# Kernel tuning notes

Hardware: AMD Instinct MI355X
Metric: run time of the kernel (lower is better)

## Reference

```python
import jax, jax.numpy as jnp
import numpy as np
import math

B, S, E = 2, 2048, 1024
H, HD = 16, 64  # num_heads, head_size


def setup_inputs() -> dict:
    key = jax.random.key(0)
    ks = jax.random.split(key, 9)
    sc = 1.0 / math.sqrt(HD)
    return {
        "x": jax.random.normal(ks[0], (B, S, E), dtype=jnp.float32),
        "Wq_w": jax.random.normal(ks[1], (HD, HD), dtype=jnp.float32) * sc,
        "Wq_b": jax.random.normal(ks[2], (HD,), dtype=jnp.float32) * 0.02,
        "Wk_w": jax.random.normal(ks[3], (HD, HD), dtype=jnp.float32) * sc,
        "Wk_b": jax.random.normal(ks[4], (HD,), dtype=jnp.float32) * 0.02,
        "Wv_w": jax.random.normal(ks[5], (HD, HD), dtype=jnp.float32) * sc,
        "Wv_b": jax.random.normal(ks[6], (HD,), dtype=jnp.float32) * 0.02,
        "proj_w": jax.random.normal(ks[7], (E, E), dtype=jnp.float32) * (1.0 / math.sqrt(E)),
        "proj_b": jax.random.normal(ks[8], (E,), dtype=jnp.float32) * 0.02,
    }


def reference(x, Wq_w, Wq_b, Wk_w, Wk_b, Wv_w, Wv_b, proj_w, proj_b):
    b, s, _ = x.shape
    xh = x.reshape(b, s, H, HD)  # split heads; QKV linears act per-head (shared weights)
    # torch Linear: y = x @ W.T + b
    q = jnp.einsum('bshd,ed->bhse', xh, Wq_w) + Wq_b  # [B,H,S,HD]
    k = jnp.einsum('bshd,ed->bhse', xh, Wk_w) + Wk_b
    v = jnp.einsum('bshd,ed->bhse', xh, Wv_w) + Wv_b
    scores = jnp.einsum('bhqd,bhkd->bhqk', q, k) / math.sqrt(HD)
    causal = jnp.tril(jnp.ones((s, s), dtype=bool))
    scores = jnp.where(causal, scores, jnp.float32(-1e20))
    attn = jax.nn.softmax(scores, axis=-1)  # attn_dropout p=0 (eval)
    out = jnp.einsum('bhqk,bhkd->bqhd', attn, v).reshape(b, s, H * HD)
    out = out @ proj_w.T + proj_b  # resid_dropout p=0 (eval)
    return out
```

## Files before the change

kernel.cpp:

```cpp
#include <hip/hip_runtime.h>
#include <hip/hip_bf16.h>

#define B_ 2
#define S_ 2048
#define E_ 1024
#define H_ 16
#define HD_ 64
#define T_ (B_ * S_)

typedef short bf16x8 __attribute__((ext_vector_type(8)));
typedef short bf16x4 __attribute__((ext_vector_type(4)));
typedef float f32x4 __attribute__((ext_vector_type(4)));

__device__ __forceinline__ short f2bf(float f) {
  union { float f; unsigned u; } v;
  v.f = f;
  unsigned r = v.u + 0x7fffu + ((v.u >> 16) & 1u);
  return (short)(r >> 16);
}

__device__ __forceinline__ void gll16(const void* g, void* l) {
  __builtin_amdgcn_global_load_lds(
      (const __attribute__((address_space(1))) unsigned int*)g,
      (__attribute__((address_space(3))) unsigned int*)l, 16, 0, 0);
}


__global__ __launch_bounds__(256) void qkv_conv_kernel(
    const float* __restrict__ x,
    const float* __restrict__ wq, const float* __restrict__ bq,
    const float* __restrict__ wk, const float* __restrict__ bk,
    const float* __restrict__ wv, const float* __restrict__ bv,
    short* __restrict__ Q, short* __restrict__ KV,
    const float* __restrict__ pw, short* __restrict__ pwb) {
  const int tid = threadIdx.x;
  if (blockIdx.x >= 512) {
    int i = ((blockIdx.x - 512) * 256 + tid) * 4;
    float4 f = *(const float4*)(pw + i);
    bf16x4 o;
    o[0] = f2bf(f.x); o[1] = f2bf(f.y); o[2] = f2bf(f.z); o[3] = f2bf(f.w);
    *(bf16x4*)(pwb + i) = o;
    return;
  }
  __shared__ short Xs[64][136];
  __shared__ short Ws[192][72];
  __shared__ short Qt[64][68], Kt[64][68], Vt[64][68];

  const int bid = blockIdx.x;
  const int tb = bid >> 3, hg = bid & 7;
  const int s0 = (tb * 64) & (S_ - 1);
  const int kt = s0 >> 6;
  const int bb = (tb * 64) >> 11;
  const int wave = tid >> 6, lane = tid & 63;
  const int lrow = lane & 15, quad = lane >> 4;

#pragma unroll
  for (int i = 0; i < 8; i++) {
    int c = tid + 256 * i;
    int row = c >> 5, col4 = c & 31;
    float4 f = *(const float4*)(x + ((long)(tb * 64 + row)) * E_ + hg * 128 + col4 * 4);
    bf16x4 o;
    o[0] = f2bf(f.x); o[1] = f2bf(f.y); o[2] = f2bf(f.z); o[3] = f2bf(f.w);
    *(bf16x4*)&Xs[row][col4 * 4] = o;
  }
#pragma unroll
  for (int m = 0; m < 3; m++) {
    const float* w = (m == 0) ? wq : (m == 1) ? wk : wv;
#pragma unroll
    for (int i = 0; i < 4; i++) {
      int c = tid + 256 * i;
      int row = m * 64 + (c >> 4), col = (c & 15) * 4;
      float4 f = *(const float4*)(w + (long)c * 4);
      bf16x4 o;
      o[0] = f2bf(f.x); o[1] = f2bf(f.y); o[2] = f2bf(f.z); o[3] = f2bf(f.w);
      *(bf16x4*)&Ws[row][col] = o;
    }
  }
  float bias[12];
#pragma unroll
  for (int nb = 0; nb < 12; nb++) {
    int sel = nb >> 2;
    int e = ((nb & 3) * 16) + lrow;
    bias[nb] = ((sel == 0) ? bq : (sel == 1) ? bk : bv)[e];
  }
  __syncthreads();

  bf16x8 bf0[12], bf1[12];
#pragma unroll
  for (int nb = 0; nb < 12; nb++) {
    bf0[nb] = *(bf16x8*)&Ws[nb * 16 + lrow][quad * 8];
    bf1[nb] = *(bf16x8*)&Ws[nb * 16 + lrow][32 + quad * 8];
  }

  const float QSCALE = 0.125f * 1.44269504089f;
  for (int hl = 0; hl < 2; hl++) {
    const int h = hg * 2 + hl;
    bf16x8 a0 = *(bf16x8*)&Xs[wave * 16 + lrow][hl * 64 + quad * 8];
    bf16x8 a1 = *(bf16x8*)&Xs[wave * 16 + lrow][hl * 64 + 32 + quad * 8];
#pragma unroll
    for (int nb = 0; nb < 12; nb++) {
      f32x4 acc = {0.f, 0.f, 0.f, 0.f};
      acc = __builtin_amdgcn_mfma_f32_16x16x32_bf16(a0, bf0[nb], acc, 0, 0, 0);
      acc = __builtin_amdgcn_mfma_f32_16x16x32_bf16(a1, bf1[nb], acc, 0, 0, 0);
      const int sel = nb >> 2;
      const float scale = (sel == 0) ? QSCALE : 1.0f;
      short (*ct)[68] = (sel == 0) ? Qt : (sel == 1) ? Kt : Vt;
#pragma unroll
      for (int r = 0; r < 4; r++) {
        ct[wave * 16 + quad * 4 + r][(nb & 3) * 16 + lrow] =
            f2bf((acc[r] + bias[nb]) * scale);
      }
    }
    __syncthreads();

    const int bh = bb * H_ + h;
    short* Qg = Q + ((long)bh * S_ + s0) * HD_;
    short* Tg = KV + ((long)(bh * 32 + kt)) * 8192;
#pragma unroll
    for (int i = 0; i < 2; i++) {
      int c = tid + 256 * i;
      int row = c >> 3, col = (c & 7) * 8;
      *(bf16x8*)(Qg + (long)row * HD_ + col) = *(bf16x8*)&Qt[row][col];
    }
#pragma unroll
    for (int u = 0; u < 4; u++) {
      int fid = tid + 256 * u;
      bf16x8 val;
      int lane2 = fid & 63;
      int quad2 = lane2 >> 4, lrow2 = lane2 & 15;
      if (u < 2) {
        int g = fid >> 6;
        int nb = g >> 1, half = g & 1;
        val = *(bf16x8*)&Kt[nb * 16 + lrow2][half * 32 + quad2 * 8];
      } else {
        int g = (fid >> 6) & 7;
        int p2 = g >> 2, db = g & 3;
#pragma unroll
        for (int j = 0; j < 8; j++) {
          int key = (2 * p2 + (j >> 2)) * 16 + quad2 * 4 + (j & 3);
          val[j] = Vt[key][db * 16 + lrow2];
        }
      }
      *(bf16x8*)(Tg + fid * 8) = val;
    }
    __syncthreads();
  }
}

__global__ __launch_bounds__(256, 2) void attn_kernel(
    const short* __restrict__ Q, const short* __restrict__ KV,
    short* __restrict__ O ) {
  __shared__ __align__(16) short L[2][16384];

  const int tid = threadIdx.x;
  const int bid = blockIdx.x;
  const int bh = bid & 31;
  const int pr = bid >> 5;
  const int g = (pr < 8) ? (15 - pr) : (pr - 8);
  const int b = bh >> 4, h = bh & 15;
  const long qbase = ((long)bh) << 17;

  const int wave = tid >> 6, lane = tid & 63;
  const int lrow = lane & 15, quad = lane >> 4;
  const int qgA = g * 128 + wave * 16 + lrow;
  const int qgB = qgA + 64;

  const short* qpA = Q + qbase + (long)qgA * HD_;
  const short* qpB = Q + qbase + (long)qgB * HD_;
  bf16x8 qfA0 = *(const bf16x8*)(qpA + quad * 8);
  bf16x8 qfA1 = *(const bf16x8*)(qpA + 32 + quad * 8);
  bf16x8 qfB0 = *(const bf16x8*)(qpB + quad * 8);
  bf16x8 qfB1 = *(const bf16x8*)(qpB + 32 + quad * 8);

  const char* Tg = (const char*)(KV + ((long)bh * 32) * 8192);

  auto STAGE = [&](int sup, int buf) {
    const char* gt = Tg + (long)sup * 32768;
#pragma unroll
    for (int u = 0; u < 8; u++) {
      const int chunk = u * 4 + wave;
      gll16(gt + chunk * 1024 + lane * 16, &L[buf][chunk * 512]);
    }
  };

  f32x4 OA[4], OB[4];
#pragma unroll
  for (int db = 0; db < 4; db++) {
    OA[db] = f32x4{0.f, 0.f, 0.f, 0.f};
    OB[db] = f32x4{0.f, 0.f, 0.f, 0.f};
  }
  float lsA = 0.f, lsB = 0.f;

  const int nsup = g + 1;
  STAGE(0, 0);
  for (int it = 0; it < nsup; it++) {
    const int buf = it & 1;
    __syncthreads();
    if (it + 1 < nsup) STAGE(it + 1, buf ^ 1);
    const bool last = (it == nsup - 1);

#pragma unroll
    for (int s2 = 0; s2 < 2; s2++) {
      const short* Lb = &L[buf][s2 * 8192];
      const bool doA = !(last && s2 == 1);

      bf16x8 kf[8];
#pragma unroll
      for (int g2 = 0; g2 < 8; g2++)
        kf[g2] = *(bf16x8*)&Lb[g2 * 512 + lane * 8];

      f32x4 scA[4], scB[4];
#pragma unroll
      for (int nb = 0; nb < 4; nb++) {
        f32x4 cb = {0.f, 0.f, 0.f, 0.f};
        cb = __builtin_amdgcn_mfma_f32_16x16x32_bf16(kf[2 * nb], qfB0, cb, 0, 0, 0);
        cb = __builtin_amdgcn_mfma_f32_16x16x32_bf16(kf[2 * nb + 1], qfB1, cb, 0, 0, 0);
        scB[nb] = cb;
      }
      if (doA) {
#pragma unroll
        for (int nb = 0; nb < 4; nb++) {
          f32x4 ca = {0.f, 0.f, 0.f, 0.f};
          ca = __builtin_amdgcn_mfma_f32_16x16x32_bf16(kf[2 * nb], qfA0, ca, 0, 0, 0);
          ca = __builtin_amdgcn_mfma_f32_16x16x32_bf16(kf[2 * nb + 1], qfA1, ca, 0, 0, 0);
          scA[nb] = ca;
        }
      }

      bf16x8 vf[8];
#pragma unroll
      for (int g2 = 0; g2 < 8; g2++)
        vf[g2] = *(bf16x8*)&Lb[4096 + g2 * 512 + lane * 8];

      if (last && s2 == 0) {
        const int k0 = 2 * g * 64;
#pragma unroll
        for (int nb = 0; nb < 4; nb++) {
          int kgl = k0 + nb * 16 + quad * 4;
#pragma unroll
          for (int r = 0; r < 4; r++)
            if (kgl + r > qgA) scA[nb][r] = -1e30f;
        }
      }
      if (last && s2 == 1) {
        const int k0 = (2 * g + 1) * 64;
#pragma unroll
        for (int nb = 0; nb < 4; nb++) {
          int kgl = k0 + nb * 16 + quad * 4;
#pragma unroll
          for (int r = 0; r < 4; r++)
            if (kgl + r > qgB) scB[nb][r] = -1e30f;
        }
      }

      bf16x4 pfA[4], pfB[4];
#pragma unroll
      for (int nb = 0; nb < 4; nb++) {
        unsigned ub[4];
#pragma unroll
        for (int r = 0; r < 4; r++) {
          float p = __builtin_amdgcn_exp2f(scB[nb][r]);
          lsB += p;
          ub[r] = __float_as_uint(p);
        }
        union { unsigned q[2]; bf16x4 v; } pk;
        pk.q[0] = __builtin_amdgcn_perm(ub[1], ub[0], 0x07060302u);
        pk.q[1] = __builtin_amdgcn_perm(ub[3], ub[2], 0x07060302u);
        pfB[nb] = pk.v;
      }
      if (doA) {
#pragma unroll
        for (int nb = 0; nb < 4; nb++) {
          unsigned ua[4];
#pragma unroll
          for (int r = 0; r < 4; r++) {
            float p = __builtin_amdgcn_exp2f(scA[nb][r]);
            lsA += p;
            ua[r] = __float_as_uint(p);
          }
          union { unsigned q[2]; bf16x4 v; } pk;
          pk.q[0] = __builtin_amdgcn_perm(ua[1], ua[0], 0x07060302u);
          pk.q[1] = __builtin_amdgcn_perm(ua[3], ua[2], 0x07060302u);
          pfA[nb] = pk.v;
        }
      }

#pragma unroll
      for (int p2 = 0; p2 < 2; p2++) {
#pragma unroll
        for (int db = 0; db < 4; db++) {
          bf16x8 vv = vf[p2 * 4 + db];
          bf16x4 vlo = {vv[0], vv[1], vv[2], vv[3]};
          bf16x4 vhi = {vv[4], vv[5], vv[6], vv[7]};
          OB[db] = __builtin_amdgcn_mfma_f32_16x16x16bf16_1k(vlo, pfB[2 * p2], OB[db], 0, 0, 0);
          OB[db] = __builtin_amdgcn_mfma_f32_16x16x16bf16_1k(vhi, pfB[2 * p2 + 1], OB[db], 0, 0, 0);
          if (doA) {
            OA[db] = __builtin_amdgcn_mfma_f32_16x16x16bf16_1k(vlo, pfA[2 * p2], OA[db], 0, 0, 0);
            OA[db] = __builtin_amdgcn_mfma_f32_16x16x16bf16_1k(vhi, pfA[2 * p2 + 1], OA[db], 0, 0, 0);
          }
        }
      }
    }
  }

  lsA += __shfl_xor(lsA, 16);
  lsA += __shfl_xor(lsA, 32);
  lsB += __shfl_xor(lsB, 16);
  lsB += __shfl_xor(lsB, 32);
  const float invA = 1.f / lsA, invB = 1.f / lsB;
  short* oA = O + ((long)b * S_ + qgA) * E_ + h * HD_;
  short* oB = O + ((long)b * S_ + qgB) * E_ + h * HD_;
#pragma unroll
  for (int db = 0; db < 4; db++) {
    bf16x4 oa, ob;
#pragma unroll
    for (int r = 0; r < 4; r++) {
      oa[r] = f2bf(OA[db][r] * invA);
      ob[r] = f2bf(OB[db][r] * invB);
    }
    *(bf16x4*)(oA + db * 16 + quad * 4) = oa;
    *(bf16x4*)(oB + db * 16 + quad * 4) = ob;
  }
}

__global__ __launch_bounds__(256) void proj_kernel(
    const short* __restrict__ A, const short* __restrict__ W,
    const float* __restrict__ bias, float* __restrict__ out) {
  __shared__ short As[2][128][72];
  __shared__ short Bs[2][64][72];
  const int tid = threadIdx.x;
  const int bid = blockIdx.x;
  const int m0 = (bid >> 4) * 128;
  const int n0 = (bid & 15) * 64;
  const int wave = tid >> 6, lane = tid & 63;
  const int wm = wave >> 1, wn = wave & 1;
  const int lrow = lane & 15, quad = lane >> 4;

  const int sr = tid >> 3, sc = (tid & 7) * 8;

  bf16x8 ar[4], br[2];
  auto LDR = [&](int k0) {
#pragma unroll
    for (int u = 0; u < 4; u++) {
      int cid = tid + 256 * u;
      int row = cid >> 3, col = (cid & 7) * 8;
      ar[u] = *(const bf16x8*)(A + (long)(m0 + row) * E_ + k0 + col);
    }
#pragma unroll
    for (int u = 0; u < 2; u++) {
      int cid = tid + 256 * u;
      int row = cid >> 3, col = (cid & 7) * 8;
      br[u] = *(const bf16x8*)(W + (long)(n0 + row) * E_ + k0 + col);
    }
  };

  f32x4 acc[4][2];
#pragma unroll
  for (int i = 0; i < 4; i++)
#pragma unroll
    for (int j = 0; j < 2; j++) acc[i][j] = f32x4{0.f, 0.f, 0.f, 0.f};

  LDR(0);
  for (int kk = 0; kk < 16; kk++) {
    const int buf = kk & 1;
#pragma unroll
    for (int u = 0; u < 4; u++) {
      int cid = tid + 256 * u;
      *(bf16x8*)&As[buf][cid >> 3][(cid & 7) * 8] = ar[u];
    }
#pragma unroll
    for (int u = 0; u < 2; u++) {
      int cid = tid + 256 * u;
      *(bf16x8*)&Bs[buf][cid >> 3][(cid & 7) * 8] = br[u];
    }
    __syncthreads();
    if (kk < 15) LDR((kk + 1) * 64);

#pragma unroll
    for (int kh = 0; kh < 2; kh++) {
      bf16x8 af[4], bfr[2];
#pragma unroll
      for (int i = 0; i < 4; i++)
        af[i] = *(bf16x8*)&As[buf][wm * 64 + i * 16 + lrow][kh * 32 + quad * 8];
#pragma unroll
      for (int j = 0; j < 2; j++)
        bfr[j] = *(bf16x8*)&Bs[buf][wn * 32 + j * 16 + lrow][kh * 32 + quad * 8];
#pragma unroll
      for (int i = 0; i < 4; i++)
#pragma unroll
        for (int j = 0; j < 2; j++)
          acc[i][j] = __builtin_amdgcn_mfma_f32_16x16x32_bf16(af[i], bfr[j], acc[i][j], 0, 0, 0);
    }
  }

#pragma unroll
  for (int j = 0; j < 2; j++) {
    int col = n0 + wn * 32 + j * 16 + lrow;
    float bv = bias[col];
#pragma unroll
    for (int i = 0; i < 4; i++) {
#pragma unroll
      for (int r = 0; r < 4; r++) {
        int row = m0 + wm * 64 + i * 16 + quad * 4 + r;
        out[(long)row * E_ + col] = acc[i][j][r] + bv;
      }
    }
  }
}

extern "C" void kernel_launch(void* const* d_in, const int* in_sizes, int n_in,
                              void* d_out, int out_size, void* d_ws, size_t ws_size,
                              hipStream_t stream) {
  const float* x  = (const float*)d_in[0];
  const float* wq = (const float*)d_in[1];
  const float* bq = (const float*)d_in[2];
  const float* wk = (const float*)d_in[3];
  const float* bk = (const float*)d_in[4];
  const float* wv = (const float*)d_in[5];
  const float* bv = (const float*)d_in[6];
  const float* pw = (const float*)d_in[7];
  const float* pb = (const float*)d_in[8];
  float* out = (float*)d_out;

  char* ws = (char*)d_ws;
  short* Qb = (short*)(ws);
  short* KVb = (short*)(ws + (size_t)8 * 1024 * 1024);
  short* AO = (short*)(ws + (size_t)24 * 1024 * 1024);
  short* PW = (short*)(ws + (size_t)32 * 1024 * 1024);

  qkv_conv_kernel<<<dim3(512 + 1024), dim3(256), 0, stream>>>(
      x, wq, bq, wk, bk, wv, bv, Qb, KVb, pw, PW);
  attn_kernel<<<dim3(16 * 32), dim3(256), 0, stream>>>(Qb, KVb, AO);
  proj_kernel<<<dim3(32 * 16), dim3(256), 0, stream>>>(AO, PW, pb, out);
}
```

Measured before the change: 133.9 us.

## Use direct global-to-LDS loads with XOR swizzle in proj GEMM; add MFMA priority hints

The projection GEMM now stages A and W tiles straight into LDS with global_load_lds, skipping the register round-trip. An XOR swizzle on 16-byte chunks replaces the padded layout to avoid LDS bank conflicts, and the fragment reads use the matching swizzled column. In the attention kernel, s_setprio raises wave priority around the QK and PV MFMA blocks so waves doing matrix math get issue preference. Risks are possible wait/sync ordering issues with async LDS loads, and priority hints that may do nothing.

```diff
diff --git a/kernel.cpp b/kernel.cpp
--- a/kernel.cpp
+++ b/kernel.cpp
@@ -210,6 +210,7 @@
         kf[g2] = *(bf16x8*)&Lb[g2 * 512 + lane * 8];
 
       f32x4 scA[4], scB[4];
+      __builtin_amdgcn_s_setprio(1);
 #pragma unroll
       for (int nb = 0; nb < 4; nb++) {
         f32x4 cb = {0.f, 0.f, 0.f, 0.f};
@@ -226,6 +227,7 @@
           scA[nb] = ca;
         }
       }
+      __builtin_amdgcn_s_setprio(0);
 
       bf16x8 vf[8];
 #pragma unroll
@@ -285,6 +287,7 @@
         }
       }
 
+      __builtin_amdgcn_s_setprio(1);
 #pragma unroll
       for (int p2 = 0; p2 < 2; p2++) {
 #pragma unroll
@@ -300,6 +303,7 @@
           }
         }
       }
+      __builtin_amdgcn_s_setprio(0);
     }
   }
 
@@ -326,8 +330,8 @@
 __global__ __launch_bounds__(256) void proj_kernel(
     const short* __restrict__ A, const short* __restrict__ W,
     const float* __restrict__ bias, float* __restrict__ out) {
-  __shared__ short As[2][128][72];
-  __shared__ short Bs[2][64][72];
+  __shared__ __align__(16) short As[2][128][64];
+  __shared__ __align__(16) short Bs[2][64][64];
   const int tid = threadIdx.x;
   const int bid = blockIdx.x;
   const int m0 = (bid >> 4) * 128;
@@ -336,21 +340,20 @@
   const int wm = wave >> 1, wn = wave & 1;
   const int lrow = lane & 15, quad = lane >> 4;
 
-  const int sr = tid >> 3, sc = (tid & 7) * 8;
-
-  bf16x8 ar[4], br[2];
-  auto LDR = [&](int k0) {
+  auto STAGE = [&](int k0, int bufi) {
 #pragma unroll
     for (int u = 0; u < 4; u++) {
-      int cid = tid + 256 * u;
-      int row = cid >> 3, col = (cid & 7) * 8;
-      ar[u] = *(const bf16x8*)(A + (long)(m0 + row) * E_ + k0 + col);
+      int d = u * 256 + tid;
+      int row = d >> 3, c = d & 7;
+      gll16(A + (long)(m0 + row) * E_ + k0 + ((c ^ (row & 7)) * 8),
+            (short*)As[bufi] + (u * 256 + wave * 64) * 8);
     }
 #pragma unroll
     for (int u = 0; u < 2; u++) {
-      int cid = tid + 256 * u;
-      int row = cid >> 3, col = (cid & 7) * 8;
-      br[u] = *(const bf16x8*)(W + (long)(n0 + row) * E_ + k0 + col);
+      int d = u * 256 + tid;
+      int row = d >> 3, c = d & 7;
+      gll16(W + (long)(n0 + row) * E_ + k0 + ((c ^ (row & 7)) * 8),
+            (short*)Bs[bufi] + (u * 256 + wave * 64) * 8);
     }
   };
 
@@ -360,31 +363,25 @@
 #pragma unroll
     for (int j = 0; j < 2; j++) acc[i][j] = f32x4{0.f, 0.f, 0.f, 0.f};
 
-  LDR(0);
+  STAGE(0, 0);
   for (int kk = 0; kk < 16; kk++) {
     const int buf = kk & 1;
-#pragma unroll
-    for (int u = 0; u < 4; u++) {
-      int cid = tid + 256 * u;
-      *(bf16x8*)&As[buf][cid >> 3][(cid & 7) * 8] = ar[u];
-    }
-#pragma unroll
-    for (int u = 0; u < 2; u++) {
-      int cid = tid + 256 * u;
-      *(bf16x8*)&Bs[buf][cid >> 3][(cid & 7) * 8] = br[u];
-    }
     __syncthreads();
-    if (kk < 15) LDR((kk + 1) * 64);
+    if (kk < 15) STAGE((kk + 1) * 64, buf ^ 1);
 
 #pragma unroll
     for (int kh = 0; kh < 2; kh++) {
       bf16x8 af[4], bfr[2];
 #pragma unroll
-      for (int i = 0; i < 4; i++)
-        af[i] = *(bf16x8*)&As[buf][wm * 64 + i * 16 + lrow][kh * 32 + quad * 8];
-#pragma unroll
-      for (int j = 0; j < 2; j++)
-        bfr[j] = *(bf16x8*)&Bs[buf][wn * 32 + j * 16 + lrow][kh * 32 + quad * 8];
+      for (int i = 0; i < 4; i++) {
+        int ra = wm * 64 + i * 16 + lrow;
+        af[i] = *(bf16x8*)&As[buf][ra][((kh * 4 + quad) ^ (lrow & 7)) * 8];
+      }
+#pragma unroll
+      for (int j = 0; j < 2; j++) {
+        int rb = wn * 32 + j * 16 + lrow;
+        bfr[j] = *(bf16x8*)&Bs[buf][rb][((kh * 4 + quad) ^ (lrow & 7)) * 8];
+      }
 #pragma unroll
       for (int i = 0; i < 4; i++)
 #pragma unroll
```

Measured after the change: 135.8 us. Within noise of the previous version (+1.4%).
